# Kernel tuning notes

Hardware: AMD Instinct MI355X
Metric: run time of the kernel (lower is better)

Reference implementation:

```python
import jax, jax.numpy as jnp
import numpy as np

N_HEAD = 16
HEAD_SIZE = 64  # n_embd // n_head = 1024 // 16


def setup_inputs() -> dict:
    key = jax.random.key(0)
    k1, k2 = jax.random.split(key)
    B, T, C = 2, 2048, 1024
    x = jax.random.normal(k1, (B, T, C), dtype=jnp.float32)
    w_attn = jax.random.normal(k2, (C, 3 * C), dtype=jnp.float32) * (C ** -0.5)
    b_attn = jnp.zeros((3 * C,), dtype=jnp.float32)
    return {"x": x, "w_attn": w_attn, "b_attn": b_attn}


def reference(x, w_attn, b_attn):
    B, T, C = x.shape
    qkv = x @ w_attn + b_attn  # [B, T, 3C]
    q, k, v = jnp.split(qkv, 3, axis=-1)
    # [B, T, H, D] -> [B, H, T, D]
    def heads(t):
        return t.reshape(B, T, N_HEAD, HEAD_SIZE).transpose(0, 2, 1, 3)
    q, k, v = heads(q), heads(k), heads(v)
    scale = HEAD_SIZE ** -0.5
    wei = jnp.einsum('bhqd,bhkd->bhqk', q, k) * scale  # [B, H, T, T]
    causal = jnp.tril(jnp.ones((T, T), dtype=bool))
    wei = jnp.where(causal, wei, -jnp.inf)
    wei = jax.nn.softmax(wei, axis=-1)
    out = jnp.einsum('bhqk,bhkd->bhqd', wei, v)  # [B, H, T, D]
    out = out.transpose(0, 2, 1, 3).reshape(B, T, C)
    return out
```

## Files before the change

### kernel.cpp

```cpp
#include <hip/hip_runtime.h>
#include <hip/hip_bf16.h>

#define BSZ 2
#define SEQ 2048
#define CDIM 1024
#define NHEAD 16
#define HDIM 64
#define M_GEMM (BSZ * SEQ)
#define N_GEMM (3 * CDIM)
#define K_GEMM CDIM
#define QK_PITCH (2 * CDIM)

typedef __attribute__((ext_vector_type(8))) short short8;
typedef __attribute__((ext_vector_type(4))) short short4v;
typedef __attribute__((ext_vector_type(4))) float f32x4;

__device__ __forceinline__ short bf16_rn(float f) {
    unsigned u = __builtin_bit_cast(unsigned, f);
    u += 0x7FFF + ((u >> 16) & 1);
    return (short)(u >> 16);
}

__device__ __forceinline__ void gl2lds16(const short* g, short* l) {
    __builtin_amdgcn_global_load_lds(
        (const __attribute__((address_space(1))) unsigned int*)g,
        (__attribute__((address_space(3))) unsigned int*)l, 16, 0, 0);
}

__global__ __launch_bounds__(256) void cvt_fused(const float* __restrict__ X,
                                                 const float* __restrict__ W,
                                                 short* __restrict__ Xb,
                                                 short* __restrict__ WT) {
    const int tid = threadIdx.x;
    if (blockIdx.x < 2048) {
        size_t idx = ((size_t)blockIdx.x * 256 + tid) * 8;
        float4 a = *(const float4*)&X[idx];
        float4 b = *(const float4*)&X[idx + 4];
        short8 o;
        o[0] = bf16_rn(a.x); o[1] = bf16_rn(a.y); o[2] = bf16_rn(a.z); o[3] = bf16_rn(a.w);
        o[4] = bf16_rn(b.x); o[5] = bf16_rn(b.y); o[6] = bf16_rn(b.z); o[7] = bf16_rn(b.w);
        *(short8*)&Xb[idx] = o;
        return;
    }
    __shared__ short T[64][72];
    const int bid = blockIdx.x - 2048;
    const int n0 = (bid % 48) * 64;
    const int k0 = (bid / 48) * 64;
#pragma unroll
    for (int pass = 0; pass < 4; ++pass) {
        int i = pass * 256 + tid;
        int kr = i >> 4;
        int n4 = i & 15;
        float4 v = *(const float4*)&W[(size_t)(k0 + kr) * N_GEMM + n0 + n4 * 4];
        T[n4 * 4 + 0][kr] = bf16_rn(v.x);
        T[n4 * 4 + 1][kr] = bf16_rn(v.y);
        T[n4 * 4 + 2][kr] = bf16_rn(v.z);
        T[n4 * 4 + 3][kr] = bf16_rn(v.w);
    }
    __syncthreads();
#pragma unroll
    for (int pass = 0; pass < 2; ++pass) {
        int o = pass * 256 + tid;
        int nr = o >> 3;
        int c8 = o & 7;
        *(short8*)&WT[(size_t)(n0 + nr) * K_GEMM + k0 + c8 * 8] =
            *(const short8*)&T[nr][c8 * 8];
    }
}

#define GBK 64

__global__ __launch_bounds__(256) void qkv_gemm_mfma(const short* __restrict__ A,
                                                     const short* __restrict__ Bt,
                                                     const float* __restrict__ bias,
                                                     short* __restrict__ Yqk,
                                                     short* __restrict__ Yv) {
    __shared__ short Asl[128 * GBK];
    __shared__ short Bsl[128 * GBK];

    const int tid = threadIdx.x;
    const int w = tid >> 6;
    const int l16 = tid & 15;
    const int quad = (tid & 63) >> 4;
    const int wm = w >> 1, wn = w & 1;
    const int m0 = blockIdx.y * 128;
    const int n0 = blockIdx.x * 128;

    f32x4 acc[4][4];
#pragma unroll
    for (int i = 0; i < 4; ++i)
#pragma unroll
        for (int j = 0; j < 4; ++j) acc[i][j] = (f32x4){0.f, 0.f, 0.f, 0.f};

    int arow[4], gofs[4];
#pragma unroll
    for (int p = 0; p < 4; ++p) {
        int cid = p * 256 + tid;
        arow[p] = cid >> 3;
        gofs[p] = ((cid & 7) ^ (arow[p] & 7)) * 8;
    }
    const int fsw = l16 & 7;

    for (int kt = 0; kt < K_GEMM; kt += GBK) {
        __syncthreads();
#pragma unroll
        for (int p = 0; p < 4; ++p) {
            gl2lds16(A + (size_t)(m0 + arow[p]) * K_GEMM + kt + gofs[p],
                     &Asl[(p * 256 + w * 64) * 8]);
            gl2lds16(Bt + (size_t)(n0 + arow[p]) * K_GEMM + kt + gofs[p],
                     &Bsl[(p * 256 + w * 64) * 8]);
        }
        __syncthreads();

        short8 af[4][2], bfr[4][2];
#pragma unroll
        for (int i = 0; i < 4; ++i) {
            int ra = wm * 64 + i * 16 + l16;
            int rb = wn * 64 + i * 16 + l16;
#pragma unroll
            for (int ks = 0; ks < 2; ++ks) {
                af[i][ks] = *(const short8*)&Asl[(ra * 8 + ((ks * 4 + quad) ^ fsw)) * 8];
                bfr[i][ks] = *(const short8*)&Bsl[(rb * 8 + ((ks * 4 + quad) ^ fsw)) * 8];
            }
        }
#pragma unroll
        for (int i = 0; i < 4; ++i)
#pragma unroll
            for (int j = 0; j < 4; ++j)
#pragma unroll
                for (int ks = 0; ks < 2; ++ks)
                    acc[i][j] = __builtin_amdgcn_mfma_f32_16x16x32_bf16(
                        af[i][ks], bfr[j][ks], acc[i][j], 0, 0, 0);
    }

    if (n0 >= 2 * CDIM) {
#pragma unroll
        for (int i = 0; i < 4; ++i) {
            int row0 = m0 + wm * 64 + i * 16 + quad * 4;
#pragma unroll
            for (int j = 0; j < 4; ++j) {
                int colg = n0 + wn * 64 + j * 16 + l16;
                float bb = bias[colg];
                short4v pk;
#pragma unroll
                for (int r = 0; r < 4; ++r) pk[r] = bf16_rn(acc[i][j][r] + bb);
                *(short4v*)&Yv[(size_t)(colg - 2 * CDIM) * M_GEMM + row0] = pk;
            }
        }
    } else {
        const float qs = (n0 < CDIM) ? 0.125f : 1.0f;
#pragma unroll
        for (int i = 0; i < 4; ++i)
#pragma unroll
            for (int r = 0; r < 4; ++r) {
                int row = m0 + wm * 64 + i * 16 + quad * 4 + r;
#pragma unroll
                for (int j = 0; j < 4; ++j) {
                    int colg = n0 + wn * 64 + j * 16 + l16;
                    Yqk[(size_t)row * QK_PITCH + colg] =
                        bf16_rn((acc[i][j][r] + bias[colg]) * qs);
                }
            }
    }
}

__global__ __launch_bounds__(128) void attn_mfma(const short* __restrict__ qk,
                                                 const short* __restrict__ vT,
                                                 float* __restrict__ out) {
    const int b = blockIdx.z;
    const int h = blockIdx.y;
    const int qt = gridDim.x - 1 - blockIdx.x;
    const int tid = threadIdx.x;
    const int w = tid >> 6;
    const int lane = tid & 63;
    const int quad = lane >> 4;
    const int l16 = lane & 15;
    const int q0 = qt * 64;

    __shared__ short Ks[64 * 64];
    __shared__ short Vt[64 * 64];
    __shared__ short Ps[2 * 32 * 64];

    int koff[4], voff[4];
    short *ksb[4], *vtb[4];
#pragma unroll
    for (int p = 0; p < 4; ++p) {
        int cid = p * 128 + w * 64 + lane;
        int row = cid >> 3;
        int c = (cid & 7) ^ (row & 7);
        koff[p] = row * QK_PITCH + c * 8;
        voff[p] = row * M_GEMM + c * 8;
        ksb[p] = &Ks[(p * 128 + w * 64) * 8];
        vtb[p] = &Vt[(p * 128 + w * 64) * 8];
    }

    short8 aq[2][2];
#pragma unroll
    for (int s = 0; s < 2; ++s) {
        const short* qrow =
            qk + (size_t)(b * SEQ + q0 + w * 32 + s * 16 + l16) * QK_PITCH + h * HDIM;
        aq[s][0] = *(const short8*)(qrow + quad * 8);
        aq[s][1] = *(const short8*)(qrow + 32 + quad * 8);
    }

    float l_run[2][4] = {{0.f, 0.f, 0.f, 0.f}, {0.f, 0.f, 0.f, 0.f}};
    f32x4 o_acc[2][4];
#pragma unroll
    for (int s = 0; s < 2; ++s)
#pragma unroll
        for (int dt = 0; dt < 4; ++dt) o_acc[s][dt] = (f32x4){0.f, 0.f, 0.f, 0.f};

    const short* kb0 = qk + (size_t)(b * SEQ) * QK_PITCH + CDIM + h * HDIM;
    const short* vb0 = vT + (size_t)(h * HDIM) * M_GEMM + b * SEQ;

    const int ksl = l16 & 7;
    short* PsW = &Ps[w * 2048];

    for (int kt = 0; kt <= qt; ++kt) {
        const short* kbase = kb0 + (size_t)kt * 64 * QK_PITCH;
        const short* vbase = vb0 + kt * 64;

        __syncthreads();
#pragma unroll
        for (int p = 0; p < 4; ++p) {
            gl2lds16(kbase + koff[p], ksb[p]);
            gl2lds16(vbase + voff[p], vtb[p]);
        }
        __syncthreads();

        f32x4 s0[4], s1[4];
#pragma unroll
        for (int nt = 0; nt < 4; ++nt) {
            s0[nt] = (f32x4){0.f, 0.f, 0.f, 0.f};
            s1[nt] = (f32x4){0.f, 0.f, 0.f, 0.f};
        }
#pragma unroll
        for (int ks = 0; ks < 2; ++ks)
#pragma unroll
            for (int nt = 0; nt < 4; ++nt) {
                short8 bk = *(const short8*)&Ks[(nt * 16 + l16) * 64 +
                                                ((ks * 4 + quad) ^ ksl) * 8];
                s0[nt] = __builtin_amdgcn_mfma_f32_16x16x32_bf16(aq[0][ks], bk, s0[nt], 0, 0, 0);
                s1[nt] = __builtin_amdgcn_mfma_f32_16x16x32_bf16(aq[1][ks], bk, s1[nt], 0, 0, 0);
            }

        if (kt < qt) {
#pragma unroll
            for (int s = 0; s < 2; ++s) {
                const f32x4* sr = (s == 0) ? s0 : s1;
#pragma unroll
                for (int r = 0; r < 4; ++r) {
                    const int qr = s * 16 + quad * 4 + r;
                    float lsum = 0.f;
#pragma unroll
                    for (int nt = 0; nt < 4; ++nt) {
                        float pp = __expf(sr[nt][r]);
                        lsum += pp;
                        int slot = (nt * 2 + (l16 >> 3)) ^ (qr & 7);
                        PsW[qr * 64 + slot * 8 + (l16 & 7)] = bf16_rn(pp);
                    }
                    l_run[s][r] += lsum;
                }
            }
        } else {
            const int keyb = kt * 64 + l16;
#pragma unroll
            for (int s = 0; s < 2; ++s) {
                const f32x4* sr = (s == 0) ? s0 : s1;
                const int rowg0 = q0 + w * 32 + s * 16 + quad * 4;
#pragma unroll
                for (int r = 0; r < 4; ++r) {
                    const int qr = s * 16 + quad * 4 + r;
                    float lsum = 0.f;
#pragma unroll
                    for (int nt = 0; nt < 4; ++nt) {
                        float pp = __expf(sr[nt][r]);
                        pp = ((keyb + nt * 16) > (rowg0 + r)) ? 0.f : pp;
                        lsum += pp;
                        int slot = (nt * 2 + (l16 >> 3)) ^ (qr & 7);
                        PsW[qr * 64 + slot * 8 + (l16 & 7)] = bf16_rn(pp);
                    }
                    l_run[s][r] += lsum;
                }
            }
        }

#pragma unroll
        for (int ks = 0; ks < 2; ++ks) {
            short8 ap0 = *(const short8*)&PsW[l16 * 64 + ((ks * 4 + quad) ^ ksl) * 8];
            short8 ap1 = *(const short8*)&PsW[(16 + l16) * 64 + ((ks * 4 + quad) ^ ksl) * 8];
#pragma unroll
            for (int dt = 0; dt < 4; ++dt) {
                short8 bv = *(const short8*)&Vt[(dt * 16 + l16) * 64 +
                                                ((ks * 4 + quad) ^ ksl) * 8];
                o_acc[0][dt] = __builtin_amdgcn_mfma_f32_16x16x32_bf16(ap0, bv, o_acc[0][dt], 0, 0, 0);
                o_acc[1][dt] = __builtin_amdgcn_mfma_f32_16x16x32_bf16(ap1, bv, o_acc[1][dt], 0, 0, 0);
            }
        }
    }

#pragma unroll
    for (int s = 0; s < 2; ++s)
#pragma unroll
        for (int r = 0; r < 4; ++r) {
            float l = l_run[s][r];
#pragma unroll
            for (int off = 1; off < 16; off <<= 1)
                l += __shfl_xor(l, off);
            float inv = 1.f / l;
            int row = q0 + w * 32 + s * 16 + quad * 4 + r;
            float* optr = out + (size_t)(b * SEQ + row) * CDIM + h * HDIM;
#pragma unroll
            for (int dt = 0; dt < 4; ++dt)
                optr[dt * 16 + l16] = o_acc[s][dt][r] * inv;
        }
}

extern "C" void kernel_launch(void* const* d_in, const int* in_sizes, int n_in,
                              void* d_out, int out_size, void* d_ws, size_t ws_size,
                              hipStream_t stream) {
    const float* x      = (const float*)d_in[0];
    const float* w_attn = (const float*)d_in[1];
    const float* b_attn = (const float*)d_in[2];
    float* out = (float*)d_out;

    short* qk  = (short*)d_ws;
    short* vT  = (short*)((char*)d_ws + 16777216);
    short* xb  = (short*)((char*)d_ws + 25165824);
    short* wT  = (short*)((char*)d_ws + 33554432);

    cvt_fused<<<2048 + 768, 256, 0, stream>>>(x, w_attn, xb, wT);

    dim3 g1(N_GEMM / 128, M_GEMM / 128);
    qkv_gemm_mfma<<<g1, 256, 0, stream>>>(xb, wT, b_attn, qk, vT);

    dim3 g2(SEQ / 64, NHEAD, BSZ);
    attn_mfma<<<g2, 128, 0, stream>>>(qk, vT, out);
}
```

Baseline: 187.9 us.

## Halve attention query tile to 32 rows per block for more blocks

The attention kernel now assigns 32 query rows per block (16 per wave) instead of 64, doubling the grid to SEQ/32 blocks. Each block iterates key tiles up to (q0+31)/64, masking only on the last tile. This raises parallelism and occupancy across CUs but halves reuse of each K/V tile loaded into LDS, so total K/V traffic and sync count increase.

Result: slower. 194.1 us (+3.3%).

```diff
diff --git a/kernel.cpp b/kernel.cpp
--- a/kernel.cpp
+++ b/kernel.cpp
@@ -175,17 +175,17 @@
     const int lane = tid & 63;
     const int quad = lane >> 4;
     const int l16 = lane & 15;
-    const int q0 = qt * 64;
+    const int q0 = qt * 32;
 
     __shared__ short Ks[64 * 64];
     __shared__ short Vt[64 * 64];
-    __shared__ short Ps[2 * 32 * 64];
+    __shared__ short Ps[2 * 16 * 64];
 
     int koff[4], voff[4];
     short *ksb[4], *vtb[4];
 #pragma unroll
     for (int p = 0; p < 4; ++p) {
-        int cid = p * 128 + w * 64 + lane;
+        int cid = p * 128 + tid;
         int row = cid >> 3;
         int c = (cid & 7) ^ (row & 7);
         koff[p] = row * QK_PITCH + c * 8;
@@ -194,29 +194,25 @@
         vtb[p] = &Vt[(p * 128 + w * 64) * 8];
     }
 
-    short8 aq[2][2];
-#pragma unroll
-    for (int s = 0; s < 2; ++s) {
-        const short* qrow =
-            qk + (size_t)(b * SEQ + q0 + w * 32 + s * 16 + l16) * QK_PITCH + h * HDIM;
-        aq[s][0] = *(const short8*)(qrow + quad * 8);
-        aq[s][1] = *(const short8*)(qrow + 32 + quad * 8);
-    }
-
-    float l_run[2][4] = {{0.f, 0.f, 0.f, 0.f}, {0.f, 0.f, 0.f, 0.f}};
-    f32x4 o_acc[2][4];
-#pragma unroll
-    for (int s = 0; s < 2; ++s)
-#pragma unroll
-        for (int dt = 0; dt < 4; ++dt) o_acc[s][dt] = (f32x4){0.f, 0.f, 0.f, 0.f};
-
+    const short* qrow = qk + (size_t)(b * SEQ + q0 + w * 16 + l16) * QK_PITCH + h * HDIM;
+    short8 aq[2];
+    aq[0] = *(const short8*)(qrow + quad * 8);
+    aq[1] = *(const short8*)(qrow + 32 + quad * 8);
+
+    float l_run[4] = {0.f, 0.f, 0.f, 0.f};
+    f32x4 o_acc[4];
+#pragma unroll
+    for (int dt = 0; dt < 4; ++dt) o_acc[dt] = (f32x4){0.f, 0.f, 0.f, 0.f};
+
+    const int rowg0 = q0 + w * 16 + quad * 4;
+    const int ktmax = (q0 + 31) >> 6;
     const short* kb0 = qk + (size_t)(b * SEQ) * QK_PITCH + CDIM + h * HDIM;
     const short* vb0 = vT + (size_t)(h * HDIM) * M_GEMM + b * SEQ;
 
     const int ksl = l16 & 7;
-    short* PsW = &Ps[w * 2048];
-
-    for (int kt = 0; kt <= qt; ++kt) {
+    short* PsW = &Ps[w * 1024];
+
+    for (int kt = 0; kt <= ktmax; ++kt) {
         const short* kbase = kb0 + (size_t)kt * 64 * QK_PITCH;
         const short* vbase = vb0 + kt * 64;
 
@@ -228,92 +224,75 @@
         }
         __syncthreads();
 
-        f32x4 s0[4], s1[4];
-#pragma unroll
-        for (int nt = 0; nt < 4; ++nt) {
-            s0[nt] = (f32x4){0.f, 0.f, 0.f, 0.f};
-            s1[nt] = (f32x4){0.f, 0.f, 0.f, 0.f};
-        }
-#pragma unroll
-        for (int ks = 0; ks < 2; ++ks)
-#pragma unroll
-            for (int nt = 0; nt < 4; ++nt) {
+        f32x4 s[4];
+#pragma unroll
+        for (int nt = 0; nt < 4; ++nt) s[nt] = (f32x4){0.f, 0.f, 0.f, 0.f};
+#pragma unroll
+        for (int nt = 0; nt < 4; ++nt)
+#pragma unroll
+            for (int ks = 0; ks < 2; ++ks) {
                 short8 bk = *(const short8*)&Ks[(nt * 16 + l16) * 64 +
                                                 ((ks * 4 + quad) ^ ksl) * 8];
-                s0[nt] = __builtin_amdgcn_mfma_f32_16x16x32_bf16(aq[0][ks], bk, s0[nt], 0, 0, 0);
-                s1[nt] = __builtin_amdgcn_mfma_f32_16x16x32_bf16(aq[1][ks], bk, s1[nt], 0, 0, 0);
-            }
-
-        if (kt < qt) {
-#pragma unroll
-            for (int s = 0; s < 2; ++s) {
-                const f32x4* sr = (s == 0) ? s0 : s1;
-#pragma unroll
-                for (int r = 0; r < 4; ++r) {
-                    const int qr = s * 16 + quad * 4 + r;
-                    float lsum = 0.f;
-#pragma unroll
-                    for (int nt = 0; nt < 4; ++nt) {
-                        float pp = __expf(sr[nt][r]);
-                        lsum += pp;
-                        int slot = (nt * 2 + (l16 >> 3)) ^ (qr & 7);
-                        PsW[qr * 64 + slot * 8 + (l16 & 7)] = bf16_rn(pp);
-                    }
-                    l_run[s][r] += lsum;
+                s[nt] = __builtin_amdgcn_mfma_f32_16x16x32_bf16(aq[ks], bk, s[nt], 0, 0, 0);
+            }
+
+        if (kt < ktmax) {
+#pragma unroll
+            for (int r = 0; r < 4; ++r) {
+                const int qr = quad * 4 + r;
+                float lsum = 0.f;
+#pragma unroll
+                for (int nt = 0; nt < 4; ++nt) {
+                    float pp = __expf(s[nt][r]);
+                    lsum += pp;
+                    int slot = (nt * 2 + (l16 >> 3)) ^ (qr & 7);
+                    PsW[qr * 64 + slot * 8 + (l16 & 7)] = bf16_rn(pp);
                 }
+                l_run[r] += lsum;
             }
         } else {
             const int keyb = kt * 64 + l16;
 #pragma unroll
-            for (int s = 0; s < 2; ++s) {
-                const f32x4* sr = (s == 0) ? s0 : s1;
-                const int rowg0 = q0 + w * 32 + s * 16 + quad * 4;
-#pragma unroll
-                for (int r = 0; r < 4; ++r) {
-                    const int qr = s * 16 + quad * 4 + r;
-                    float lsum = 0.f;
-#pragma unroll
-                    for (int nt = 0; nt < 4; ++nt) {
-                        float pp = __expf(sr[nt][r]);
-                        pp = ((keyb + nt * 16) > (rowg0 + r)) ? 0.f : pp;
-                        lsum += pp;
-                        int slot = (nt * 2 + (l16 >> 3)) ^ (qr & 7);
-                        PsW[qr * 64 + slot * 8 + (l16 & 7)] = bf16_rn(pp);
-                    }
-                    l_run[s][r] += lsum;
+            for (int r = 0; r < 4; ++r) {
+                const int qr = quad * 4 + r;
+                const int rowg = rowg0 + r;
+                float lsum = 0.f;
+#pragma unroll
+                for (int nt = 0; nt < 4; ++nt) {
+                    float pp = __expf(s[nt][r]);
+                    pp = ((keyb + nt * 16) > rowg) ? 0.f : pp;
+                    lsum += pp;
+                    int slot = (nt * 2 + (l16 >> 3)) ^ (qr & 7);
+                    PsW[qr * 64 + slot * 8 + (l16 & 7)] = bf16_rn(pp);
                 }
-            }
-        }
-
-#pragma unroll
-        for (int ks = 0; ks < 2; ++ks) {
-            short8 ap0 = *(const short8*)&PsW[l16 * 64 + ((ks * 4 + quad) ^ ksl) * 8];
-            short8 ap1 = *(const short8*)&PsW[(16 + l16) * 64 + ((ks * 4 + quad) ^ ksl) * 8];
-#pragma unroll
-            for (int dt = 0; dt < 4; ++dt) {
+                l_run[r] += lsum;
+            }
+        }
+
+#pragma unroll
+        for (int dt = 0; dt < 4; ++dt)
+#pragma unroll
+            for (int ks = 0; ks < 2; ++ks) {
+                short8 ap = *(const short8*)&PsW[l16 * 64 + ((ks * 4 + quad) ^ ksl) * 8];
                 short8 bv = *(const short8*)&Vt[(dt * 16 + l16) * 64 +
                                                 ((ks * 4 + quad) ^ ksl) * 8];
-                o_acc[0][dt] = __builtin_amdgcn_mfma_f32_16x16x32_bf16(ap0, bv, o_acc[0][dt], 0, 0, 0);
-                o_acc[1][dt] = __builtin_amdgcn_mfma_f32_16x16x32_bf16(ap1, bv, o_acc[1][dt], 0, 0, 0);
-            }
-        }
-    }
-
-#pragma unroll
-    for (int s = 0; s < 2; ++s)
-#pragma unroll
-        for (int r = 0; r < 4; ++r) {
-            float l = l_run[s][r];
-#pragma unroll
-            for (int off = 1; off < 16; off <<= 1)
-                l += __shfl_xor(l, off);
-            float inv = 1.f / l;
-            int row = q0 + w * 32 + s * 16 + quad * 4 + r;
-            float* optr = out + (size_t)(b * SEQ + row) * CDIM + h * HDIM;
-#pragma unroll
-            for (int dt = 0; dt < 4; ++dt)
-                optr[dt * 16 + l16] = o_acc[s][dt][r] * inv;
-        }
+                o_acc[dt] = __builtin_amdgcn_mfma_f32_16x16x32_bf16(ap, bv, o_acc[dt], 0, 0, 0);
+            }
+    }
+
+#pragma unroll
+    for (int r = 0; r < 4; ++r) {
+        float l = l_run[r];
+#pragma unroll
+        for (int off = 1; off < 16; off <<= 1)
+            l += __shfl_xor(l, off);
+        float inv = 1.f / l;
+        int row = q0 + w * 16 + quad * 4 + r;
+        float* optr = out + (size_t)(b * SEQ + row) * CDIM + h * HDIM;
+#pragma unroll
+        for (int dt = 0; dt < 4; ++dt)
+            optr[dt * 16 + l16] = o_acc[dt][r] * inv;
+    }
 }
 
 extern "C" void kernel_launch(void* const* d_in, const int* in_sizes, int n_in,
@@ -334,6 +313,6 @@
     dim3 g1(N_GEMM / 128, M_GEMM / 128);
     qkv_gemm_mfma<<<g1, 256, 0, stream>>>(xb, wT, b_attn, qk, vT);
 
-    dim3 g2(SEQ / 64, NHEAD, BSZ);
+    dim3 g2(SEQ / 32, NHEAD, BSZ);
     attn_mfma<<<g2, 128, 0, stream>>>(qk, vT, out);
 }
```

## Double-buffer K/V tiles and pair causal query tiles per attention block

Applied to the files above, without the earlier changes.

The attention kernel now keeps two LDS buffers for K and V. It issues the async global-to-LDS load for the next key tile before computing on the current one, leaving a single barrier per iteration. Each block now handles two query tiles, one from the long end and one from the short end of the causal triangle, so every block does the same amount of work and the grid is halved. The trade-off is twice the LDS for K/V and half as many resident blocks, which lowers the number of waves available to hide latency.

Result: no change. 187.5 us (-0.2%).

```diff
diff --git a/kernel.cpp b/kernel.cpp
--- a/kernel.cpp
+++ b/kernel.cpp
@@ -169,151 +169,167 @@
                                                  float* __restrict__ out) {
     const int b = blockIdx.z;
     const int h = blockIdx.y;
-    const int qt = gridDim.x - 1 - blockIdx.x;
     const int tid = threadIdx.x;
     const int w = tid >> 6;
     const int lane = tid & 63;
     const int quad = lane >> 4;
     const int l16 = lane & 15;
-    const int q0 = qt * 64;
-
-    __shared__ short Ks[64 * 64];
-    __shared__ short Vt[64 * 64];
+
+    __shared__ short Ks[2][64 * 64];
+    __shared__ short Vt[2][64 * 64];
     __shared__ short Ps[2 * 32 * 64];
 
-    int koff[4], voff[4];
-    short *ksb[4], *vtb[4];
+    int koff[4], voff[4], ldso[4];
 #pragma unroll
     for (int p = 0; p < 4; ++p) {
-        int cid = p * 128 + w * 64 + lane;
+        int cid = p * 128 + tid;
         int row = cid >> 3;
         int c = (cid & 7) ^ (row & 7);
         koff[p] = row * QK_PITCH + c * 8;
         voff[p] = row * M_GEMM + c * 8;
-        ksb[p] = &Ks[(p * 128 + w * 64) * 8];
-        vtb[p] = &Vt[(p * 128 + w * 64) * 8];
-    }
-
-    short8 aq[2][2];
-#pragma unroll
-    for (int s = 0; s < 2; ++s) {
-        const short* qrow =
-            qk + (size_t)(b * SEQ + q0 + w * 32 + s * 16 + l16) * QK_PITCH + h * HDIM;
-        aq[s][0] = *(const short8*)(qrow + quad * 8);
-        aq[s][1] = *(const short8*)(qrow + 32 + quad * 8);
-    }
-
-    float l_run[2][4] = {{0.f, 0.f, 0.f, 0.f}, {0.f, 0.f, 0.f, 0.f}};
-    f32x4 o_acc[2][4];
-#pragma unroll
-    for (int s = 0; s < 2; ++s)
-#pragma unroll
-        for (int dt = 0; dt < 4; ++dt) o_acc[s][dt] = (f32x4){0.f, 0.f, 0.f, 0.f};
+        ldso[p] = (p * 128 + w * 64) * 8;
+    }
 
     const short* kb0 = qk + (size_t)(b * SEQ) * QK_PITCH + CDIM + h * HDIM;
     const short* vb0 = vT + (size_t)(h * HDIM) * M_GEMM + b * SEQ;
-
     const int ksl = l16 & 7;
     short* PsW = &Ps[w * 2048];
 
-    for (int kt = 0; kt <= qt; ++kt) {
-        const short* kbase = kb0 + (size_t)kt * 64 * QK_PITCH;
-        const short* vbase = vb0 + kt * 64;
-
+    const int qts[2] = {(SEQ / 64 - 1) - (int)blockIdx.x, (int)blockIdx.x};
+
+#pragma unroll 1
+    for (int ph = 0; ph < 2; ++ph) {
+        const int qt = qts[ph];
+        const int q0 = qt * 64;
+
+        short8 aq[2][2];
+#pragma unroll
+        for (int s = 0; s < 2; ++s) {
+            const short* qrow =
+                qk + (size_t)(b * SEQ + q0 + w * 32 + s * 16 + l16) * QK_PITCH + h * HDIM;
+            aq[s][0] = *(const short8*)(qrow + quad * 8);
+            aq[s][1] = *(const short8*)(qrow + 32 + quad * 8);
+        }
+
+        float l_run[2][4] = {{0.f, 0.f, 0.f, 0.f}, {0.f, 0.f, 0.f, 0.f}};
+        f32x4 o_acc[2][4];
+#pragma unroll
+        for (int s = 0; s < 2; ++s)
+#pragma unroll
+            for (int dt = 0; dt < 4; ++dt) o_acc[s][dt] = (f32x4){0.f, 0.f, 0.f, 0.f};
+
+#pragma unroll
+        for (int p = 0; p < 4; ++p) {
+            gl2lds16(kb0 + koff[p], &Ks[0][ldso[p]]);
+            gl2lds16(vb0 + voff[p], &Vt[0][ldso[p]]);
+        }
         __syncthreads();
-#pragma unroll
-        for (int p = 0; p < 4; ++p) {
-            gl2lds16(kbase + koff[p], ksb[p]);
-            gl2lds16(vbase + voff[p], vtb[p]);
-        }
-        __syncthreads();
-
-        f32x4 s0[4], s1[4];
-#pragma unroll
-        for (int nt = 0; nt < 4; ++nt) {
-            s0[nt] = (f32x4){0.f, 0.f, 0.f, 0.f};
-            s1[nt] = (f32x4){0.f, 0.f, 0.f, 0.f};
-        }
-#pragma unroll
-        for (int ks = 0; ks < 2; ++ks)
+
+        for (int kt = 0; kt <= qt; ++kt) {
+            const int cur = kt & 1;
+
+            if (kt < qt) {
+                const short* kbase = kb0 + (size_t)(kt + 1) * 64 * QK_PITCH;
+                const short* vbase = vb0 + (kt + 1) * 64;
+#pragma unroll
+                for (int p = 0; p < 4; ++p) {
+                    gl2lds16(kbase + koff[p], &Ks[cur ^ 1][ldso[p]]);
+                    gl2lds16(vbase + voff[p], &Vt[cur ^ 1][ldso[p]]);
+                }
+            }
+
+            const short* KsC = Ks[cur];
+            const short* VtC = Vt[cur];
+
+            f32x4 s0[4], s1[4];
 #pragma unroll
             for (int nt = 0; nt < 4; ++nt) {
-                short8 bk = *(const short8*)&Ks[(nt * 16 + l16) * 64 +
-                                                ((ks * 4 + quad) ^ ksl) * 8];
-                s0[nt] = __builtin_amdgcn_mfma_f32_16x16x32_bf16(aq[0][ks], bk, s0[nt], 0, 0, 0);
-                s1[nt] = __builtin_amdgcn_mfma_f32_16x16x32_bf16(aq[1][ks], bk, s1[nt], 0, 0, 0);
-            }
-
-        if (kt < qt) {
-#pragma unroll
-            for (int s = 0; s < 2; ++s) {
-                const f32x4* sr = (s == 0) ? s0 : s1;
-#pragma unroll
-                for (int r = 0; r < 4; ++r) {
-                    const int qr = s * 16 + quad * 4 + r;
-                    float lsum = 0.f;
-#pragma unroll
-                    for (int nt = 0; nt < 4; ++nt) {
-                        float pp = __expf(sr[nt][r]);
-                        lsum += pp;
-                        int slot = (nt * 2 + (l16 >> 3)) ^ (qr & 7);
-                        PsW[qr * 64 + slot * 8 + (l16 & 7)] = bf16_rn(pp);
+                s0[nt] = (f32x4){0.f, 0.f, 0.f, 0.f};
+                s1[nt] = (f32x4){0.f, 0.f, 0.f, 0.f};
+            }
+#pragma unroll
+            for (int ks = 0; ks < 2; ++ks)
+#pragma unroll
+                for (int nt = 0; nt < 4; ++nt) {
+                    short8 bk = *(const short8*)&KsC[(nt * 16 + l16) * 64 +
+                                                     ((ks * 4 + quad) ^ ksl) * 8];
+                    s0[nt] = __builtin_amdgcn_mfma_f32_16x16x32_bf16(aq[0][ks], bk, s0[nt], 0, 0, 0);
+                    s1[nt] = __builtin_amdgcn_mfma_f32_16x16x32_bf16(aq[1][ks], bk, s1[nt], 0, 0, 0);
+                }
+
+            if (kt < qt) {
+#pragma unroll
+                for (int s = 0; s < 2; ++s) {
+                    const f32x4* sr = (s == 0) ? s0 : s1;
+#pragma unroll
+                    for (int r = 0; r < 4; ++r) {
+                        const int qr = s * 16 + quad * 4 + r;
+                        float lsum = 0.f;
+#pragma unroll
+                        for (int nt = 0; nt < 4; ++nt) {
+                            float pp = __expf(sr[nt][r]);
+                            lsum += pp;
+                            int slot = (nt * 2 + (l16 >> 3)) ^ (qr & 7);
+                            PsW[qr * 64 + slot * 8 + (l16 & 7)] = bf16_rn(pp);
+                        }
+                        l_run[s][r] += lsum;
                     }
-                    l_run[s][r] += lsum;
-                }
-            }
-        } else {
-            const int keyb = kt * 64 + l16;
-#pragma unroll
-            for (int s = 0; s < 2; ++s) {
-                const f32x4* sr = (s == 0) ? s0 : s1;
-                const int rowg0 = q0 + w * 32 + s * 16 + quad * 4;
-#pragma unroll
-                for (int r = 0; r < 4; ++r) {
-                    const int qr = s * 16 + quad * 4 + r;
-                    float lsum = 0.f;
-#pragma unroll
-                    for (int nt = 0; nt < 4; ++nt) {
-                        float pp = __expf(sr[nt][r]);
-                        pp = ((keyb + nt * 16) > (rowg0 + r)) ? 0.f : pp;
-                        lsum += pp;
-                        int slot = (nt * 2 + (l16 >> 3)) ^ (qr & 7);
-                        PsW[qr * 64 + slot * 8 + (l16 & 7)] = bf16_rn(pp);
+                }
+            } else {
+                const int keyb = kt * 64 + l16;
+#pragma unroll
+                for (int s = 0; s < 2; ++s) {
+                    const f32x4* sr = (s == 0) ? s0 : s1;
+                    const int rowg0 = q0 + w * 32 + s * 16 + quad * 4;
+#pragma unroll
+                    for (int r = 0; r < 4; ++r) {
+                        const int qr = s * 16 + quad * 4 + r;
+                        float lsum = 0.f;
+#pragma unroll
+                        for (int nt = 0; nt < 4; ++nt) {
+                            float pp = __expf(sr[nt][r]);
+                            pp = ((keyb + nt * 16) > (rowg0 + r)) ? 0.f : pp;
+                            lsum += pp;
+                            int slot = (nt * 2 + (l16 >> 3)) ^ (qr & 7);
+                            PsW[qr * 64 + slot * 8 + (l16 & 7)] = bf16_rn(pp);
+                        }
+                        l_run[s][r] += lsum;
                     }
-                    l_run[s][r] += lsum;
-                }
-            }
-        }
-
-#pragma unroll
-        for (int ks = 0; ks < 2; ++ks) {
-            short8 ap0 = *(const short8*)&PsW[l16 * 64 + ((ks * 4 + quad) ^ ksl) * 8];
-            short8 ap1 = *(const short8*)&PsW[(16 + l16) * 64 + ((ks * 4 + quad) ^ ksl) * 8];
-#pragma unroll
-            for (int dt = 0; dt < 4; ++dt) {
-                short8 bv = *(const short8*)&Vt[(dt * 16 + l16) * 64 +
-                                                ((ks * 4 + quad) ^ ksl) * 8];
-                o_acc[0][dt] = __builtin_amdgcn_mfma_f32_16x16x32_bf16(ap0, bv, o_acc[0][dt], 0, 0, 0);
-                o_acc[1][dt] = __builtin_amdgcn_mfma_f32_16x16x32_bf16(ap1, bv, o_acc[1][dt], 0, 0, 0);
-            }
-        }
-    }
-
-#pragma unroll
-    for (int s = 0; s < 2; ++s)
-#pragma unroll
-        for (int r = 0; r < 4; ++r) {
-            float l = l_run[s][r];
-#pragma unroll
-            for (int off = 1; off < 16; off <<= 1)
-                l += __shfl_xor(l, off);
-            float inv = 1.f / l;
-            int row = q0 + w * 32 + s * 16 + quad * 4 + r;
-            float* optr = out + (size_t)(b * SEQ + row) * CDIM + h * HDIM;
-#pragma unroll
-            for (int dt = 0; dt < 4; ++dt)
-                optr[dt * 16 + l16] = o_acc[s][dt][r] * inv;
-        }
+                }
+            }
+
+#pragma unroll
+            for (int ks = 0; ks < 2; ++ks) {
+                short8 ap0 = *(const short8*)&PsW[l16 * 64 + ((ks * 4 + quad) ^ ksl) * 8];
+                short8 ap1 = *(const short8*)&PsW[(16 + l16) * 64 + ((ks * 4 + quad) ^ ksl) * 8];
+#pragma unroll
+                for (int dt = 0; dt < 4; ++dt) {
+                    short8 bv = *(const short8*)&VtC[(dt * 16 + l16) * 64 +
+                                                     ((ks * 4 + quad) ^ ksl) * 8];
+                    o_acc[0][dt] = __builtin_amdgcn_mfma_f32_16x16x32_bf16(ap0, bv, o_acc[0][dt], 0, 0, 0);
+                    o_acc[1][dt] = __builtin_amdgcn_mfma_f32_16x16x32_bf16(ap1, bv, o_acc[1][dt], 0, 0, 0);
+                }
+            }
+
+            __syncthreads();
+        }
+
+#pragma unroll
+        for (int s = 0; s < 2; ++s)
+#pragma unroll
+            for (int r = 0; r < 4; ++r) {
+                float l = l_run[s][r];
+#pragma unroll
+                for (int off = 1; off < 16; off <<= 1)
+                    l += __shfl_xor(l, off);
+                float inv = 1.f / l;
+                int row = q0 + w * 32 + s * 16 + quad * 4 + r;
+                float* optr = out + (size_t)(b * SEQ + row) * CDIM + h * HDIM;
+#pragma unroll
+                for (int dt = 0; dt < 4; ++dt)
+                    optr[dt * 16 + l16] = o_acc[s][dt][r] * inv;
+            }
+    }
 }
 
 extern "C" void kernel_launch(void* const* d_in, const int* in_sizes, int n_in,
@@ -334,6 +350,6 @@
     dim3 g1(N_GEMM / 128, M_GEMM / 128);
     qkv_gemm_mfma<<<g1, 256, 0, stream>>>(xb, wT, b_attn, qk, vT);
 
-    dim3 g2(SEQ / 64, NHEAD, BSZ);
+    dim3 g2(SEQ / 128, NHEAD, BSZ);
     attn_mfma<<<g2, 128, 0, stream>>>(qk, vT, out);
 }
```
